# Performance work log

Hardware: AMD Instinct MI355X
Metric: run time of the kernel (lower is better)

## Reference

```python
import jax, jax.numpy as jnp
import numpy as np

N, T, CIN = 40000, 32, 8
VW = 64          # back_voxelwise_channels
P = 16           # v2b_maxvoxels (voxels stacked per BEV cell)
BEV_H, BEV_W = 496, 432
EPS = 1e-5


def _bn(key, shape):
    # returns stacked (gamma, beta, running_mean, running_var) along axis -2
    k1, k2, k3 = jax.random.split(key, 3)
    g = 1.0 + 0.1 * jax.random.normal(k1, shape, jnp.float32)
    b = 0.1 * jax.random.normal(k2, shape, jnp.float32)
    m = 0.1 * jax.random.normal(k3, shape, jnp.float32)
    v = jnp.ones(shape, jnp.float32)
    return jnp.stack([g, b, m, v], axis=-2)


def setup_inputs() -> dict:
    key = jax.random.key(0)
    ks = jax.random.split(key, 20)
    features = jax.random.normal(ks[0], (N, T, CIN), jnp.float32)
    cy = jax.random.randint(ks[1], (N, 1), 0, BEV_H)
    cx = jax.random.randint(ks[2], (N, 1), 0, BEV_W)
    coors = jnp.concatenate([cy, cx], axis=1).astype(jnp.int32)
    num_voxels = jax.random.randint(ks[3], (N,), 1, T + 1).astype(jnp.int32)

    def w(k, o, i):
        return jax.random.normal(k, (o, i), jnp.float32) / float(np.sqrt(i))

    return dict(
        features=features, coors=coors, num_voxels=num_voxels,
        vfe1_W=w(ks[4], 8, CIN), vfe1_bn=_bn(ks[5], (8,)),
        vfe2_W=w(ks[6], 32, 16), vfe2_bn=_bn(ks[7], (32,)),
        vfe3_W=w(ks[8], 64, 64), vfe3_bn=_bn(ks[9], (64,)),
        vfe4_W=w(ks[10], 64, 64), vfe4_bn=_bn(ks[11], (64,)),
        bfe1_W=jax.random.normal(ks[12], (16, P, P), jnp.float32) / float(np.sqrt(P)),
        bfe1_bn=_bn(ks[13], (16, P)),
        bfe2_W=jax.random.normal(ks[14], (16, 2, P), jnp.float32) / float(np.sqrt(P)),
        bfe2_bn=_bn(ks[15], (16, 2)),
        bfe3_W=w(ks[16], 128, 128), bfe3_bn=_bn(ks[17], (128,)),
    )


def _forward(features, vfe1_W, vfe1_bn, vfe2_W, vfe2_bn, vfe3_W, vfe3_bn,
             vfe4_W, vfe4_bn, bfe1_W, bfe1_bn, bfe2_W, bfe2_bn, bfe3_W, bfe3_bn,
             coors, num_voxels):
    n, t = features.shape[0], features.shape[1]
    f32 = features.dtype
    mask = (jnp.arange(t)[None, :] < num_voxels[:, None]).astype(f32)[..., None]  # [N,T,1]

    def fe(x, W, bn):  # Linear (no bias) + BatchNorm1d (eval) + Mish
        g, b, m, v = bn
        y = x @ W.T
        y = (y - m) * jax.lax.rsqrt(v + EPS) * g + b
        return y * jnp.tanh(jax.nn.softplus(y))

    def vfe(x, W, bn):  # pointwise FE, max-pool over points, concat
        p = fe(x, W, bn)
        agg = jnp.max(p, axis=1, keepdims=True)
        return jnp.concatenate([p, jnp.broadcast_to(agg, p.shape)], axis=2)

    x1 = vfe(features, vfe1_W, vfe1_bn)           # [N,T,16]
    x2 = vfe(x1, vfe2_W, vfe2_bn) * mask          # [N,T,64]
    x3 = fe(x2, vfe3_W, vfe3_bn)
    x4 = fe(x3, vfe4_W, vfe4_bn) * mask + x2
    voxelwise = jnp.max(x4, axis=1)               # [N,64]

    # ---- voxel2bev: group voxels by BEV cell, stack up to P per cell ----
    cell = coors[:, 0] * BEV_W + coors[:, 1]                         # [N]
    ucell, inv = jnp.unique(cell, return_inverse=True, size=n, fill_value=BEV_H * BEV_W)
    order = jnp.argsort(inv)                                          # stable
    inv_sorted = inv[order]
    pos_sorted = jnp.arange(n) - jnp.searchsorted(inv_sorted, inv_sorted, side='left')
    slot = jnp.zeros(n, jnp.int32).at[order].set(pos_sorted.astype(jnp.int32))
    row = jnp.where(slot < P, inv, n)                                 # overflow -> dropped
    bevs = jnp.zeros((n, P, VW), f32).at[row, jnp.minimum(slot, P - 1)].set(
        voxelwise, mode='drop')                                       # [N,P,64]
    counts = jax.ops.segment_sum(jnp.ones(n, jnp.int32), inv, num_segments=n)
    numv = jnp.minimum(counts, P)
    bevcoors = jnp.stack([ucell // BEV_W, ucell % BEV_W], axis=1)     # [N,2]

    # ---- 16 grouped FE stacks over the slot dimension ----
    x0 = bevs.transpose(0, 2, 1).reshape(n, 16, 4, P)                 # [N,16,4,P]
    m2 = (jnp.arange(P)[None, :] < numv[:, None]).astype(f32)[:, None, None, :]
    y = jnp.einsum('ngip,gqp->ngiq', x0, bfe1_W)                      # [N,16,4,P]
    g1, b1, m1, v1 = (bfe1_bn[None, :, i, None, :] for i in range(4))
    y = (y - m1) * jax.lax.rsqrt(v1 + EPS) * g1 + b1
    y = y * jnp.tanh(jax.nn.softplus(y)) * m2
    z = jnp.einsum('ngip,gcp->ngic', y, bfe2_W)                       # [N,16,4,2]
    g2, b2, m2b, v2 = (bfe2_bn[None, :, i, None, :] for i in range(4))
    z = (z - m2b) * jax.lax.rsqrt(v2 + EPS) * g2 + b2
    z = z * jnp.tanh(jax.nn.softplus(z))
    # torch cat along dim=-1 then view -> layout [N, 4, 16, 2] flattened
    x17 = z.transpose(0, 2, 1, 3).reshape(n, 128)
    x18 = fe(x17, bfe3_W, bfe3_bn)
    x19 = fe(x18, bfe3_W, bfe3_bn)   # original applies bfe3 twice (bfe4 unused)

    bevmap = jnp.zeros((BEV_H, BEV_W, 128), f32).at[
        bevcoors[:, 0], bevcoors[:, 1]].set(x19, mode='drop')
    return bevmap.transpose(2, 1, 0)                                  # [128, W, H]


def reference(features, coors, num_voxels, vfe1_W, vfe1_bn, vfe2_W, vfe2_bn,
              vfe3_W, vfe3_bn, vfe4_W, vfe4_bn, bfe1_W, bfe1_bn, bfe2_W, bfe2_bn,
              bfe3_W, bfe3_bn):
    return _forward(features, vfe1_W, vfe1_bn, vfe2_W, vfe2_bn, vfe3_W, vfe3_bn,
                    vfe4_W, vfe4_bn, bfe1_W, bfe1_bn, bfe2_W, bfe2_bn,
                    bfe3_W, bfe3_bn, coors, num_voxels)
```

## Files before the change

kernel.cpp:

```cpp
#include <hip/hip_runtime.h>

#define BEVW 432
#define BEVH 496
#define NCELL (BEVW*BEVH)
#define NVOX  40000
#define EPSB  1e-5f

typedef float f32x2 __attribute__((ext_vector_type(2)));
typedef float f32x4 __attribute__((ext_vector_type(4)));
typedef unsigned int u32x4 __attribute__((ext_vector_type(4)));
typedef short bf16x8 __attribute__((ext_vector_type(8)));

#define REP8_0(M)  M(0) M(1) M(2) M(3) M(4) M(5) M(6) M(7)
#define REP8_8(M)  M(8) M(9) M(10) M(11) M(12) M(13) M(14) M(15)
#define REP8_16(M) M(16) M(17) M(18) M(19) M(20) M(21) M(22) M(23)
#define REP8_24(M) M(24) M(25) M(26) M(27) M(28) M(29) M(30) M(31)
#define REP16_0(M)  REP8_0(M)  REP8_8(M)
#define REP32_0(M) REP16_0(M) REP8_16(M) REP8_24(M)


__device__ __forceinline__ float mishf(float y) {
    float e = __expf(fminf(y, 40.f));
    float n = e * (e + 2.f);
    return y * n * __builtin_amdgcn_rcpf(n + 2.f);
}

template <int CTRL>
__device__ __forceinline__ float dppmaxf(float a) {
    int p = __builtin_amdgcn_update_dpp(0, __float_as_int(a), CTRL, 0xF, 0xF, true);
    return fmaxf(a, __int_as_float(p));
}
#define WMAX32(a) { \
    a = dppmaxf<0xB1>(a); \
    a = dppmaxf<0x4E>(a); \
    a = dppmaxf<0x141>(a); \
    a = dppmaxf<0x140>(a); \
    a = fmaxf(a, __int_as_float(__builtin_amdgcn_ds_swizzle(__float_as_int(a), 0x401F))); }

__device__ __forceinline__ bf16x8 mkbf8(uint a, uint b, uint c, uint d) {
    u32x4 t = {a, b, c, d};
    return __builtin_bit_cast(bf16x8, t);
}

__device__ __forceinline__ uint splitbf(float x) {
    uint ux = __float_as_uint(x);
    uint rh = (ux + 0x7FFFu + ((ux >> 16) & 1u)) & 0xFFFF0000u;
    float lof = x - __uint_as_float(rh);
    uint ul = __float_as_uint(lof);
    uint rl = (ul + 0x7FFFu + ((ul >> 16) & 1u)) >> 16;
    return (rh >> 16) | (rl << 16);
}

__global__ __launch_bounds__(256) void setup_kernel(
    const float* __restrict__ vbn1, const float* __restrict__ vbn2,
    const float* __restrict__ vbn3, const float* __restrict__ vbn4,
    const float* __restrict__ bbn1, const float* __restrict__ bbn2,
    const float* __restrict__ bbn3, const float* __restrict__ W4,
    float* __restrict__ fold, ushort* __restrict__ w4fh, ushort* __restrict__ w4fl)
{
    int tid = threadIdx.x;
    if (tid < 8)  { float s = vbn1[tid]/sqrtf(vbn1[24+tid]+EPSB);  fold[tid]      = s; fold[8+tid]   = vbn1[8+tid]  - vbn1[16+tid]*s; }
    if (tid < 32) { float s = vbn2[tid]/sqrtf(vbn2[96+tid]+EPSB);  fold[16+tid]   = s; fold[48+tid]  = vbn2[32+tid] - vbn2[64+tid]*s; }
    if (tid < 64) { float s = vbn3[tid]/sqrtf(vbn3[192+tid]+EPSB); fold[80+tid]   = s; fold[144+tid] = vbn3[64+tid] - vbn3[128+tid]*s; }
    if (tid < 64) { float s = vbn4[tid]/sqrtf(vbn4[192+tid]+EPSB); fold[208+tid]  = s; fold[272+tid] = vbn4[64+tid] - vbn4[128+tid]*s; }
    if (tid < 128){ float s = bbn3[tid]/sqrtf(bbn3[384+tid]+EPSB); fold[336+tid]  = s; fold[464+tid] = bbn3[128+tid]- bbn3[256+tid]*s; }
    { int g = tid >> 4, q = tid & 15;
      const float* b = bbn1 + g*64;
      float s = b[q]/sqrtf(b[48+q]+EPSB);
      fold[592+tid] = s; fold[848+tid] = b[16+q] - b[32+q]*s; }
    if (tid < 32) { int g = tid >> 1, c = tid & 1;
      const float* b = bbn2 + g*8;
      float s = b[c]/sqrtf(b[6+c]+EPSB);
      fold[1104+tid] = s; fold[1136+tid] = b[2+c] - b[4+c]*s; }

    for (int i = tid; i < 4096; i += 256) {
        int j = i & 7, ln = (i >> 3) & 63, nt = (i >> 9) & 3, kc = i >> 11;
        int n = (ln & 15) + nt*16;
        int k = kc*32 + (ln >> 4)*8 + j;
        float val = W4[n*64 + k];
        uint ux = __float_as_uint(val);
        uint rh = (ux + 0x7FFFu + ((ux >> 16) & 1u)) & 0xFFFF0000u;
        float lof = val - __uint_as_float(rh);
        uint ul = __float_as_uint(lof);
        uint rl = (ul + 0x7FFFu + ((ul >> 16) & 1u)) >> 16;
        w4fh[i] = (ushort)(rh >> 16);
        w4fl[i] = (ushort)rl;
    }
}

#define PAIRS(M) M(0,0,1) M(1,2,3) M(2,4,5) M(3,6,7) M(4,8,9) M(5,10,11) \
  M(6,12,13) M(7,14,15) M(8,16,17) M(9,18,19) M(10,20,21) M(11,22,23) \
  M(12,24,25) M(13,26,27) M(14,28,29) M(15,30,31)

#define MF3(D, AH, AL, BH, BL) \
    D = __builtin_amdgcn_mfma_f32_16x16x32_bf16(AL, BH, D, 0, 0, 0); \
    D = __builtin_amdgcn_mfma_f32_16x16x32_bf16(AH, BL, D, 0, 0, 0); \
    D = __builtin_amdgcn_mfma_f32_16x16x32_bf16(AH, BH, D, 0, 0, 0);

__global__ __launch_bounds__(256, 3) void vfe_kernel(
    const float* __restrict__ feat, const int* __restrict__ coors,
    const int* __restrict__ nvx,
    const float* __restrict__ W1, const float* __restrict__ W2,
    const float* __restrict__ W3,
    const ushort* __restrict__ w4fh, const ushort* __restrict__ w4fl,
    const float* __restrict__ fold,
    float* __restrict__ voxelwise, int* __restrict__ cnt,
    int* __restrict__ list, int* __restrict__ nact, int* __restrict__ act)
{
    __shared__ char ldsbuf[4*8704];
    int tid = threadIdx.x;
    int lane = tid & 63;
    int wv = tid >> 6;
    int quad = lane >> 4;
    int v = blockIdx.x * 8 + (tid >> 5);
    int vA = blockIdx.x * 8 + 2*wv;
    int t = tid & 31;
    uint*  x3w  = (uint*)(ldsbuf + wv*8704);
    float* xw   = (float*)x3w;
    float* aggL = (float*)(ldsbuf + wv*8704 + 8448);

    const float* fp = feat + (v*32 + t)*8;
    float4 fa = *(const float4*)fp;
    float4 fb = *(const float4*)(fp+4);
    int numv = nvx[v];
    float maskf = (t < numv) ? 1.f : 0.f;

#define D1(o) float x1_##o; float m1_##o;
    REP8_0(D1)
#undef D1
#define FE1(o) { const float* w = W1 + (o)*8; \
    float ya = fa.x*w[0] + fa.y*w[1]; float yb = fa.z*w[2] + fa.w*w[3]; \
    float yc = fb.x*w[4] + fb.y*w[5]; float yd = fb.z*w[6] + fb.w*w[7]; \
    float yy = ((ya+yb)+(yc+yd)) * fold[(o)] + fold[8+(o)]; \
    x1_##o = mishf(yy); }
    REP8_0(FE1)
#undef FE1
#define P1(o) { float a = x1_##o; WMAX32(a); m1_##o = a; }
    REP8_0(P1)
#undef P1

    f32x2 x1p_0 = {x1_0,x1_1}, x1p_1 = {x1_2,x1_3}, x1p_2 = {x1_4,x1_5}, x1p_3 = {x1_6,x1_7};
    f32x2 m1p_0 = {m1_0,m1_1}, m1p_1 = {m1_2,m1_3}, m1p_2 = {m1_4,m1_5}, m1p_3 = {m1_6,m1_7};

#define D2(o) float x2_##o; float agg_##o;
    REP32_0(D2)
#undef D2
#define FE2(o) { const f32x2* wp = (const f32x2*)(W2 + (o)*16); \
    f32x2 sa = x1p_0*wp[0]; sa += x1p_1*wp[1]; \
    f32x2 sb = x1p_2*wp[2]; sb += x1p_3*wp[3]; \
    f32x2 sc = m1p_0*wp[4]; sc += m1p_1*wp[5]; \
    f32x2 sd = m1p_2*wp[6]; sd += m1p_3*wp[7]; \
    sa += sb; sc += sd; sa += sc; \
    float yy = (sa.x + sa.y) * fold[16+(o)] + fold[48+(o)]; \
    x2_##o = mishf(yy); }
    REP32_0(FE2)
#undef FE2
#define P2(o) { float a = x2_##o; WMAX32(a); agg_##o = a; }
    REP32_0(P2)
#undef P2

#define PX(i,a,b) f32x2 x2p_##i = {x2_##a, x2_##b}; f32x2 aggp_##i = {agg_##a, agg_##b};
    PAIRS(PX)
#undef PX

    const f32x2* wap = (const f32x2*)(W3 + t*64 + 32);
    const f32x2* wbp = (const f32x2*)(W3 + (t+32)*64 + 32);
    f32x2 yp1 = {0.f,0.f}, yp2 = {0.f,0.f};
#define YG(i) yp1 += aggp_##i * wap[i]; yp2 += aggp_##i * wbp[i];
    REP16_0(YG)
#undef YG
    float yagg1 = yp1.x + yp1.y, yagg2 = yp2.x + yp2.y;

    f32x2 maskp = {maskf, maskf};
#define MSK(i) x2p_##i *= maskp; aggp_##i *= maskp;
    REP16_0(MSK)
#undef MSK

    if (t == 0) {
        float* ag = aggL + (lane >> 5)*32;
#define AGW(i) ag[2*(i)] = aggp_##i.x; ag[2*(i)+1] = aggp_##i.y;
        REP16_0(AGW)
#undef AGW
    }

    int nA = __shfl(numv, 0);
    int nB = __shfl(numv, 32);

#define DD(i) f32x4 d_##i = {0.f,0.f,0.f,0.f};
    REP16_0(DD)
#undef DD

    for (int kc = 0; kc < 2; kc++) {
        float ysrc = kc ? yagg2 : yagg1;
        for (int o = 0; o < 32; o++) {
            int og = kc*32 + o;
            const f32x2* wp = (const f32x2*)(W3 + og*64);
            f32x2 s0 = x2p_0*wp[0];  s0 += x2p_1*wp[1];  s0 += x2p_2*wp[2];  s0 += x2p_3*wp[3];
            f32x2 s1 = x2p_4*wp[4];  s1 += x2p_5*wp[5];  s1 += x2p_6*wp[6];  s1 += x2p_7*wp[7];
            f32x2 s2 = x2p_8*wp[8];  s2 += x2p_9*wp[9];  s2 += x2p_10*wp[10]; s2 += x2p_11*wp[11];
            f32x2 s3 = x2p_12*wp[12]; s3 += x2p_13*wp[13]; s3 += x2p_14*wp[14]; s3 += x2p_15*wp[15];
            s0 += s1; s2 += s3; s0 += s2;
            float ya = __shfl(ysrc, o, 32);
            float yy = (s0.x + s0.y) + maskf * ya;
            yy = yy * fold[80+og] + fold[144+og];
            x3w[lane*33 + o] = splitbf(mishf(yy));
        }
        __syncthreads();

        const uint4* bh = (const uint4*)w4fh + (kc*4)*64 + lane;
        const uint4* bl = (const uint4*)w4fl + (kc*4)*64 + lane;

#define MFNT(D, nt) { \
    uint4 h = bh[(nt)*64]; uint4 l = bl[(nt)*64]; \
    bf16x8 Bh = mkbf8(h.x,h.y,h.z,h.w); bf16x8 Bl = mkbf8(l.x,l.y,l.z,l.w); \
    MF3(D, Ah, Al, Bh, Bl) }

#define DOMT(mt, D0, D1, D2, D3) { \
    int aoff = ((lane & 15) + 16*(mt))*33 + quad*8; \
    uint u0 = x3w[aoff+0], u1 = x3w[aoff+1], u2 = x3w[aoff+2], u3 = x3w[aoff+3]; \
    uint u4 = x3w[aoff+4], u5 = x3w[aoff+5], u6 = x3w[aoff+6], u7 = x3w[aoff+7]; \
    bf16x8 Ah = mkbf8(__builtin_amdgcn_perm(u1,u0,0x05040100), __builtin_amdgcn_perm(u3,u2,0x05040100), \
                      __builtin_amdgcn_perm(u5,u4,0x05040100), __builtin_amdgcn_perm(u7,u6,0x05040100)); \
    bf16x8 Al = mkbf8(__builtin_amdgcn_perm(u1,u0,0x07060302), __builtin_amdgcn_perm(u3,u2,0x07060302), \
                      __builtin_amdgcn_perm(u5,u4,0x07060302), __builtin_amdgcn_perm(u7,u6,0x07060302)); \
    MFNT(d_##D0, 0) MFNT(d_##D1, 1) MFNT(d_##D2, 2) MFNT(d_##D3, 3) }

        DOMT(0, 0, 1, 2, 3)
        DOMT(1, 4, 5, 6, 7)
        DOMT(2, 8, 9, 10, 11)
        DOMT(3, 12, 13, 14, 15)
#undef DOMT
#undef MFNT
        __syncthreads();
    }

#define XWR(i) xw[lane*33 + 2*(i)] = x2p_##i.x; xw[lane*33 + 2*(i)+1] = x2p_##i.y;
    REP16_0(XWR)
#undef XWR
    __syncthreads();

    int c0 = lane & 15;
    float s0f = fold[208+c0],    t0f = fold[272+c0];
    float s1f = fold[208+16+c0], t1f = fold[272+16+c0];
    float s2f = fold[208+32+c0], t2f = fold[272+32+c0];
    float s3f = fold[208+48+c0], t3f = fold[272+48+c0];
    float rA2 = aggL[c0],      rA3 = aggL[16+c0];
    float rB2 = aggL[32+c0],   rB3 = aggL[48+c0];
    float pA0=-3.4e38f, pA1=-3.4e38f, pA2=-3.4e38f, pA3=-3.4e38f;
    float pB0=-3.4e38f, pB1=-3.4e38f, pB2=-3.4e38f, pB3=-3.4e38f;

#define FTP(D, mt, nt, SS, TT, PV) { \
    int nv = ((mt) >> 1) ? nB : nA; \
    int rf = quad*4 + 16*(mt); \
    int rt = quad*4 + 16*((mt)&1); \
    int cb = c0 + 16*(nt); \
    float m0=(rt+0<nv)?1.f:0.f, m1=(rt+1<nv)?1.f:0.f, m2=(rt+2<nv)?1.f:0.f, m3=(rt+3<nv)?1.f:0.f; \
    float y0 = mishf(D.x*SS + TT)*m0 + xw[(rf+0)*33 + cb]; \
    float y1 = mishf(D.y*SS + TT)*m1 + xw[(rf+1)*33 + cb]; \
    float y2 = mishf(D.z*SS + TT)*m2 + xw[(rf+2)*33 + cb]; \
    float y3 = mishf(D.w*SS + TT)*m3 + xw[(rf+3)*33 + cb]; \
    PV = fmaxf(PV, fmaxf(fmaxf(y0,y1), fmaxf(y2,y3))); }

#define FTA(D, mt, nt, SS, TT, AG, PV) { \
    int nv = ((mt) >> 1) ? nB : nA; \
    int rt = quad*4 + 16*((mt)&1); \
    float m0=(rt+0<nv)?1.f:0.f, m1=(rt+1<nv)?1.f:0.f, m2=(rt+2<nv)?1.f:0.f, m3=(rt+3<nv)?1.f:0.f; \
    float y0 = (mishf(D.x*SS + TT) + AG)*m0; \
    float y1 = (mishf(D.y*SS + TT) + AG)*m1; \
    float y2 = (mishf(D.z*SS + TT) + AG)*m2; \
    float y3 = (mishf(D.w*SS + TT) + AG)*m3; \
    PV = fmaxf(PV, fmaxf(fmaxf(y0,y1), fmaxf(y2,y3))); }

    FTP(d_0, 0, 0, s0f, t0f, pA0)  FTP(d_1, 0, 1, s1f, t1f, pA1)
    FTA(d_2, 0, 2, s2f, t2f, rA2, pA2)  FTA(d_3, 0, 3, s3f, t3f, rA3, pA3)
    FTP(d_4, 1, 0, s0f, t0f, pA0)  FTP(d_5, 1, 1, s1f, t1f, pA1)
    FTA(d_6, 1, 2, s2f, t2f, rA2, pA2)  FTA(d_7, 1, 3, s3f, t3f, rA3, pA3)
    FTP(d_8, 2, 0, s0f, t0f, pB0)  FTP(d_9, 2, 1, s1f, t1f, pB1)
    FTA(d_10, 2, 2, s2f, t2f, rB2, pB2)  FTA(d_11, 2, 3, s3f, t3f, rB3, pB3)
    FTP(d_12, 3, 0, s0f, t0f, pB0)  FTP(d_13, 3, 1, s1f, t1f, pB1)
    FTA(d_14, 3, 2, s2f, t2f, rB2, pB2)  FTA(d_15, 3, 3, s3f, t3f, rB3, pB3)
#undef FTP
#undef FTA

#define RED(p) p = fmaxf(p, __shfl_xor(p, 16)); p = fmaxf(p, __shfl_xor(p, 32));
    RED(pA0) RED(pA1) RED(pA2) RED(pA3) RED(pB0) RED(pB1) RED(pB2) RED(pB3)
#undef RED

    if (quad == 0) {
        float* vwA = voxelwise + vA*64;
        vwA[c0] = pA0; vwA[c0+16] = pA1; vwA[c0+32] = pA2; vwA[c0+48] = pA3;
        float* vwB = voxelwise + (vA+1)*64;
        vwB[c0] = pB0; vwB[c0+16] = pB1; vwB[c0+32] = pB2; vwB[c0+48] = pB3;
    }

    if (t == 0) {
        int cell = coors[v*2] * BEVW + coors[v*2+1];
        int pos = atomicAdd(&cnt[cell], 1);
        if (pos < 16) list[cell*16 + pos] = v;
        if (pos == 0) { int k = atomicAdd(nact, 1); act[k] = cell; }
    }
}

__global__ __launch_bounds__(256) void bfe_front(
    const int* __restrict__ nact, const int* __restrict__ act,
    const int* __restrict__ cnt, const int* __restrict__ list,
    const float* __restrict__ voxelwise,
    const float* __restrict__ W1g, const float* __restrict__ W2g,
    const float* __restrict__ fold, float* __restrict__ x17g,
    int* __restrict__ idx)
{
    int n_act = *nact;
    int aidx = blockIdx.x * 4 + (threadIdx.x >> 6);
    if (aidx >= n_act) return;

    int lane = threadIdx.x & 63;
    int g = lane >> 2, ii = lane & 3;
    int cell = act[aidx];
    int numv = min(cnt[cell], 16);
    if (lane == 0) idx[cell] = aidx;

    int myidx = (lane < numv) ? list[cell*16 + lane] : (0x40000000 + lane);
    int rank = 0;
    for (int j = 0; j < numv; j++) { int vj = __shfl(myidx, j); rank += (vj < myidx) ? 1 : 0; }
    if (lane >= numv) rank = lane;
    int sorted = __builtin_amdgcn_ds_permute(rank << 2, myidx);

#define YD(q) float y_##q = 0.f;
    REP16_0(YD)
#undef YD
    for (int p = 0; p < numv; p++) {
        int sv = __shfl(sorted, p);
        float val = voxelwise[sv*64 + lane];
        const float* w = W1g + g*256 + p;
#define BF1(q) y_##q += val * w[(q)*16];
        REP16_0(BF1)
#undef BF1
    }
#define BN1(q) { float yy = y_##q * fold[592 + g*16 + (q)] + fold[848 + g*16 + (q)]; \
    yy = mishf(yy); y_##q = ((q) < numv) ? yy : 0.f; }
    REP16_0(BN1)
#undef BN1

    float z0 = 0.f, z1 = 0.f;
#define BF2(p) z0 += y_##p * W2g[g*32 + (p)]; z1 += y_##p * W2g[g*32 + 16 + (p)];
    REP16_0(BF2)
#undef BF2
    z0 = mishf(z0 * fold[1104 + g*2 + 0] + fold[1136 + g*2 + 0]);
    z1 = mishf(z1 * fold[1104 + g*2 + 1] + fold[1136 + g*2 + 1]);

    int k0 = ii*32 + g*2;
    *(float2*)(x17g + aidx*128 + k0) = make_float2(z0, z1);
}

__global__ __launch_bounds__(512, 4) void bfe3_fused(
    const int* __restrict__ nactp,
    const float* __restrict__ W3, const float* __restrict__ fold,
    float* __restrict__ x17g)
{
    __shared__ float XL[64*128];
    int tid = threadIdx.x;
    int n_act = *nactp;
    int cb = blockIdx.x * 64;

    for (int i = tid; i < 64*32; i += 512) {
        int c = i >> 5, kc = i & 31;
        float4 val = (cb + c < n_act) ? ((const float4*)x17g)[(size_t)(cb+c)*32 + kc]
                                      : make_float4(0.f,0.f,0.f,0.f);
        ((float4*)XL)[c*32 + (kc ^ (c & 31))] = val;
    }
    __syncthreads();

    int wv = __builtin_amdgcn_readfirstlane(tid >> 6);
    int c  = tid & 63;
    int ob = wv * 16;
    int cswz = c & 31;
    const float4* xrow = (const float4*)XL + c*32;
    const float4* W4p = (const float4*)W3;

#define DECLB(q) f32x2 ap_##q = {0.f, 0.f};
#define ACCB(q) { const f32x2* wp_ = (const f32x2*)(W4p + (ob+(q))*32 + kc); \
    ap_##q += xv01 * wp_[0]; ap_##q += xv23 * wp_[1]; }
#define ACTB(q) float a_##q; { float yy = (ap_##q.x + ap_##q.y) * fold[336+ob+(q)] + fold[464+ob+(q)]; a_##q = mishf(yy); }
    {
        REP16_0(DECLB)
        for (int kc = 0; kc < 32; kc++) {
            float4 xv = xrow[kc ^ cswz];
            f32x2 xv01 = {xv.x, xv.y}, xv23 = {xv.z, xv.w};
            REP16_0(ACCB)
        }
        REP16_0(ACTB)
        __syncthreads();
        ((float4*)XL)[c*32 + ((wv*4 + 0) ^ cswz)] = make_float4(a_0,  a_1,  a_2,  a_3);
        ((float4*)XL)[c*32 + ((wv*4 + 1) ^ cswz)] = make_float4(a_4,  a_5,  a_6,  a_7);
        ((float4*)XL)[c*32 + ((wv*4 + 2) ^ cswz)] = make_float4(a_8,  a_9,  a_10, a_11);
        ((float4*)XL)[c*32 + ((wv*4 + 3) ^ cswz)] = make_float4(a_12, a_13, a_14, a_15);
    }
    __syncthreads();

    {
        const float4* yrow = (const float4*)XL + c*32;
        REP16_0(DECLB)
        for (int kc = 0; kc < 32; kc++) {
            float4 xv = yrow[kc ^ cswz];
            f32x2 xv01 = {xv.x, xv.y}, xv23 = {xv.z, xv.w};
            REP16_0(ACCB)
        }
        REP16_0(ACTB)
        float4* dst = (float4*)(x17g + (size_t)(cb + c)*128 + ob);
        dst[0] = make_float4(a_0,  a_1,  a_2,  a_3);
        dst[1] = make_float4(a_4,  a_5,  a_6,  a_7);
        dst[2] = make_float4(a_8,  a_9,  a_10, a_11);
        dst[3] = make_float4(a_12, a_13, a_14, a_15);
    }
#undef DECLB
#undef ACCB
#undef ACTB
}

__global__ __launch_bounds__(512, 2) void bev_write(
    const int* __restrict__ idx, const float* __restrict__ x19c,
    float* __restrict__ out)
{
    __shared__ float XT[128*65];
    int bid = blockIdx.x;
    int cx = bid % BEVW;
    int cy0 = (bid / BEVW) << 6;
    int tid = threadIdx.x;

    int cell_l = tid >> 3;
    int chq = (tid & 7) << 4;
    int cy = cy0 + cell_l;
    float4 v0 = make_float4(0.f,0.f,0.f,0.f), v1 = v0, v2 = v0, v3 = v0;
    if (cy < BEVH) {
        int ai = idx[cy*BEVW + cx];
        if (ai >= 0) {
            const float4* src = (const float4*)(x19c + (size_t)ai*128 + chq);
            v0 = src[0]; v1 = src[1]; v2 = src[2]; v3 = src[3];
        }
    }
    float* d = XT + chq*65 + cell_l;
    d[0*65]=v0.x;  d[1*65]=v0.y;  d[2*65]=v0.z;  d[3*65]=v0.w;
    d[4*65]=v1.x;  d[5*65]=v1.y;  d[6*65]=v1.z;  d[7*65]=v1.w;
    d[8*65]=v2.x;  d[9*65]=v2.y;  d[10*65]=v2.z; d[11*65]=v2.w;
    d[12*65]=v3.x; d[13*65]=v3.y; d[14*65]=v3.z; d[15*65]=v3.w;
    __syncthreads();

    int wv2 = tid >> 6, lane = tid & 63;
    int cyw = cy0 + lane;
    if (cyw < BEVH) {
        float* op = out + cx*BEVH + cyw;
#pragma unroll
        for (int k = 0; k < 16; k++) {
            int c = (wv2 << 4) + k;
            op[(size_t)c*NCELL] = XT[c*65 + lane];
        }
    }
}

extern "C" void kernel_launch(void* const* d_in, const int* in_sizes, int n_in,
                              void* d_out, int out_size, void* d_ws, size_t ws_size,
                              hipStream_t stream) {
    const float* features = (const float*)d_in[0];
    const int*   coors    = (const int*)d_in[1];
    const int*   num_vox  = (const int*)d_in[2];
    const float* vfe1_W   = (const float*)d_in[3];
    const float* vfe1_bn  = (const float*)d_in[4];
    const float* vfe2_W   = (const float*)d_in[5];
    const float* vfe2_bn  = (const float*)d_in[6];
    const float* vfe3_W   = (const float*)d_in[7];
    const float* vfe3_bn  = (const float*)d_in[8];
    const float* vfe4_W   = (const float*)d_in[9];
    const float* vfe4_bn  = (const float*)d_in[10];
    const float* bfe1_W   = (const float*)d_in[11];
    const float* bfe1_bn  = (const float*)d_in[12];
    const float* bfe2_W   = (const float*)d_in[13];
    const float* bfe2_bn  = (const float*)d_in[14];
    const float* bfe3_W   = (const float*)d_in[15];
    const float* bfe3_bn  = (const float*)d_in[16];
    float* out = (float*)d_out;

    char* ws = (char*)d_ws;
    int*    nact      = (int*)ws;
    int*    cnt       = (int*)(ws + 256);
    int*    list      = (int*)(ws + 857600);
    float*  voxelwise = (float*)(ws + 14571008);
    int*    act       = (int*)(ws + 24811008);
    float*  x17g      = (float*)(ws + 24971008);
    float*  fold      = (float*)(ws + 45451008);
    ushort* w4fh      = (ushort*)(ws + 45455680);
    ushort* w4fl      = (ushort*)(ws + 45463872);
    int*    idx       = (int*)(ws + 45472064);

    (void)hipMemsetAsync(ws, 0, 857600, stream);
    (void)hipMemsetAsync(idx, 0xFF, (size_t)NCELL*4, stream);

    setup_kernel<<<1, 256, 0, stream>>>(vfe1_bn, vfe2_bn, vfe3_bn, vfe4_bn,
                                        bfe1_bn, bfe2_bn, bfe3_bn, vfe4_W,
                                        fold, w4fh, w4fl);
    vfe_kernel<<<NVOX/8, 256, 0, stream>>>(features, coors, num_vox,
                                           vfe1_W, vfe2_W, vfe3_W, w4fh, w4fl, fold,
                                           voxelwise, cnt, list, nact, act);
    bfe_front<<<NVOX/4, 256, 0, stream>>>(nact, act, cnt, list, voxelwise,
                                          bfe1_W, bfe2_W, fold, x17g, idx);
    bfe3_fused<<<(NVOX+63)/64, 512, 0, stream>>>(nact, bfe3_W, fold, x17g);
    bev_write<<<BEVW*8, 512, 0, stream>>>(idx, x17g, out);
}
```

Baseline: 560.5 us.

## Compute vfe3 linear layer with split-bf16 MFMA instead of scalar FMA

The vfe3 64x64 linear layer, previously scalar f32x2 FMAs per thread with a shuffle-based aggregate term, now runs as split-bf16 (hi/lo, three MFMA) matrix multiplies over the x2 and aggregate halves staged in LDS. vfe3_W is pre-split in the setup kernel, and the results feed vfe4 MFMAs directly through an LDS staging area. The residual x2 values are rebuilt from the split representation. LDS per block roughly doubles and the launch bound drops to 2 blocks per CU, which lowers occupancy. The split-bf16 reconstruction also brings small precision differences.

```diff
diff --git a/kernel.cpp b/kernel.cpp
--- a/kernel.cpp
+++ b/kernel.cpp
@@ -56,7 +56,9 @@
     const float* __restrict__ vbn3, const float* __restrict__ vbn4,
     const float* __restrict__ bbn1, const float* __restrict__ bbn2,
     const float* __restrict__ bbn3, const float* __restrict__ W4,
-    float* __restrict__ fold, ushort* __restrict__ w4fh, ushort* __restrict__ w4fl)
+    const float* __restrict__ W3g,
+    float* __restrict__ fold, ushort* __restrict__ w4fh, ushort* __restrict__ w4fl,
+    ushort* __restrict__ w3fh, ushort* __restrict__ w3fl)
 {
     int tid = threadIdx.x;
     if (tid < 8)  { float s = vbn1[tid]/sqrtf(vbn1[24+tid]+EPSB);  fold[tid]      = s; fold[8+tid]   = vbn1[8+tid]  - vbn1[16+tid]*s; }
@@ -77,14 +79,26 @@
         int j = i & 7, ln = (i >> 3) & 63, nt = (i >> 9) & 3, kc = i >> 11;
         int n = (ln & 15) + nt*16;
         int k = kc*32 + (ln >> 4)*8 + j;
-        float val = W4[n*64 + k];
-        uint ux = __float_as_uint(val);
-        uint rh = (ux + 0x7FFFu + ((ux >> 16) & 1u)) & 0xFFFF0000u;
-        float lof = val - __uint_as_float(rh);
-        uint ul = __float_as_uint(lof);
-        uint rl = (ul + 0x7FFFu + ((ul >> 16) & 1u)) >> 16;
-        w4fh[i] = (ushort)(rh >> 16);
-        w4fl[i] = (ushort)rl;
+        {
+            float val = W4[n*64 + k];
+            uint ux = __float_as_uint(val);
+            uint rh = (ux + 0x7FFFu + ((ux >> 16) & 1u)) & 0xFFFF0000u;
+            float lof = val - __uint_as_float(rh);
+            uint ul = __float_as_uint(lof);
+            uint rl = (ul + 0x7FFFu + ((ul >> 16) & 1u)) >> 16;
+            w4fh[i] = (ushort)(rh >> 16);
+            w4fl[i] = (ushort)rl;
+        }
+        {
+            float val = W3g[n*64 + k];
+            uint ux = __float_as_uint(val);
+            uint rh = (ux + 0x7FFFu + ((ux >> 16) & 1u)) & 0xFFFF0000u;
+            float lof = val - __uint_as_float(rh);
+            uint ul = __float_as_uint(lof);
+            uint rl = (ul + 0x7FFFu + ((ul >> 16) & 1u)) >> 16;
+            w3fh[i] = (ushort)(rh >> 16);
+            w3fl[i] = (ushort)rl;
+        }
     }
 }
 
@@ -97,17 +111,30 @@
     D = __builtin_amdgcn_mfma_f32_16x16x32_bf16(AH, BL, D, 0, 0, 0); \
     D = __builtin_amdgcn_mfma_f32_16x16x32_bf16(AH, BH, D, 0, 0, 0);
 
-__global__ __launch_bounds__(256, 3) void vfe_kernel(
+#define DOMTX(SRCP, BHP, BLP, mt, D0, D1, D2, D3) { \
+    const uint* ap_ = (SRCP) + ((lane & 15) + 16*(mt))*33 + quad*8; \
+    uint u0 = ap_[0], u1 = ap_[1], u2 = ap_[2], u3 = ap_[3]; \
+    uint u4 = ap_[4], u5 = ap_[5], u6 = ap_[6], u7 = ap_[7]; \
+    bf16x8 Ah = mkbf8(__builtin_amdgcn_perm(u1,u0,0x05040100), __builtin_amdgcn_perm(u3,u2,0x05040100), \
+                      __builtin_amdgcn_perm(u5,u4,0x05040100), __builtin_amdgcn_perm(u7,u6,0x05040100)); \
+    bf16x8 Al = mkbf8(__builtin_amdgcn_perm(u1,u0,0x07060302), __builtin_amdgcn_perm(u3,u2,0x07060302), \
+                      __builtin_amdgcn_perm(u5,u4,0x07060302), __builtin_amdgcn_perm(u7,u6,0x07060302)); \
+    { uint4 h = (BHP)[0];   uint4 l = (BLP)[0];   bf16x8 Bh = mkbf8(h.x,h.y,h.z,h.w), Bl = mkbf8(l.x,l.y,l.z,l.w); MF3(D0, Ah, Al, Bh, Bl) } \
+    { uint4 h = (BHP)[64];  uint4 l = (BLP)[64];  bf16x8 Bh = mkbf8(h.x,h.y,h.z,h.w), Bl = mkbf8(l.x,l.y,l.z,l.w); MF3(D1, Ah, Al, Bh, Bl) } \
+    { uint4 h = (BHP)[128]; uint4 l = (BLP)[128]; bf16x8 Bh = mkbf8(h.x,h.y,h.z,h.w), Bl = mkbf8(l.x,l.y,l.z,l.w); MF3(D2, Ah, Al, Bh, Bl) } \
+    { uint4 h = (BHP)[192]; uint4 l = (BLP)[192]; bf16x8 Bh = mkbf8(h.x,h.y,h.z,h.w), Bl = mkbf8(l.x,l.y,l.z,l.w); MF3(D3, Ah, Al, Bh, Bl) } }
+
+__global__ __launch_bounds__(256, 2) void vfe_kernel(
     const float* __restrict__ feat, const int* __restrict__ coors,
     const int* __restrict__ nvx,
     const float* __restrict__ W1, const float* __restrict__ W2,
-    const float* __restrict__ W3,
+    const ushort* __restrict__ w3fh, const ushort* __restrict__ w3fl,
     const ushort* __restrict__ w4fh, const ushort* __restrict__ w4fl,
     const float* __restrict__ fold,
     float* __restrict__ voxelwise, int* __restrict__ cnt,
     int* __restrict__ list, int* __restrict__ nact, int* __restrict__ act)
 {
-    __shared__ char ldsbuf[4*8704];
+    __shared__ char ldsbuf[4*17152];
     int tid = threadIdx.x;
     int lane = tid & 63;
     int wv = tid >> 6;
@@ -115,9 +142,8 @@
     int v = blockIdx.x * 8 + (tid >> 5);
     int vA = blockIdx.x * 8 + 2*wv;
     int t = tid & 31;
-    uint*  x3w  = (uint*)(ldsbuf + wv*8704);
-    float* xw   = (float*)x3w;
-    float* aggL = (float*)(ldsbuf + wv*8704 + 8448);
+    uint*  x2s  = (uint*)(ldsbuf + wv*17152);
+    float* aggL = (float*)(ldsbuf + wv*17152 + 16896);
 
     const float* fp = feat + (v*32 + t)*8;
     float4 fa = *(const float4*)fp;
@@ -163,14 +189,6 @@
     PAIRS(PX)
 #undef PX
 
-    const f32x2* wap = (const f32x2*)(W3 + t*64 + 32);
-    const f32x2* wbp = (const f32x2*)(W3 + (t+32)*64 + 32);
-    f32x2 yp1 = {0.f,0.f}, yp2 = {0.f,0.f};
-#define YG(i) yp1 += aggp_##i * wap[i]; yp2 += aggp_##i * wbp[i];
-    REP16_0(YG)
-#undef YG
-    float yagg1 = yp1.x + yp1.y, yagg2 = yp2.x + yp2.y;
-
     f32x2 maskp = {maskf, maskf};
 #define MSK(i) x2p_##i *= maskp; aggp_##i *= maskp;
     REP16_0(MSK)
@@ -186,60 +204,76 @@
     int nA = __shfl(numv, 0);
     int nB = __shfl(numv, 32);
 
+#define X2W(i) { \
+    x2s[lane*33 + 2*(i)]          = splitbf(x2p_##i.x); \
+    x2s[lane*33 + 2*(i)+1]        = splitbf(x2p_##i.y); \
+    x2s[2112 + lane*33 + 2*(i)]   = splitbf(aggp_##i.x); \
+    x2s[2112 + lane*33 + 2*(i)+1] = splitbf(aggp_##i.y); }
+    REP16_0(X2W)
+#undef X2W
+
+#define E_DECL(i) f32x4 e_##i = {0.f,0.f,0.f,0.f};
+    REP16_0(E_DECL)
+#undef E_DECL
+    {
+        const uint4* bh3 = (const uint4*)w3fh + lane;
+        const uint4* bl3 = (const uint4*)w3fl + lane;
+        DOMTX(x2s, bh3, bl3, 0, e_0, e_1, e_2, e_3)
+        DOMTX(x2s, bh3, bl3, 1, e_4, e_5, e_6, e_7)
+        DOMTX(x2s, bh3, bl3, 2, e_8, e_9, e_10, e_11)
+        DOMTX(x2s, bh3, bl3, 3, e_12, e_13, e_14, e_15)
+    }
+    {
+        const uint4* bh3 = (const uint4*)w3fh + 256 + lane;
+        const uint4* bl3 = (const uint4*)w3fl + 256 + lane;
+        const uint* sp = x2s + 2112;
+        DOMTX(sp, bh3, bl3, 0, e_0, e_1, e_2, e_3)
+        DOMTX(sp, bh3, bl3, 1, e_4, e_5, e_6, e_7)
+        DOMTX(sp, bh3, bl3, 2, e_8, e_9, e_10, e_11)
+        DOMTX(sp, bh3, bl3, 3, e_12, e_13, e_14, e_15)
+    }
+
+    int c0 = lane & 15;
+    uint* x3st = x2s + 2112;
 #define DD(i) f32x4 d_##i = {0.f,0.f,0.f,0.f};
     REP16_0(DD)
 #undef DD
 
-    for (int kc = 0; kc < 2; kc++) {
-        float ysrc = kc ? yagg2 : yagg1;
-        for (int o = 0; o < 32; o++) {
-            int og = kc*32 + o;
-            const f32x2* wp = (const f32x2*)(W3 + og*64);
-            f32x2 s0 = x2p_0*wp[0];  s0 += x2p_1*wp[1];  s0 += x2p_2*wp[2];  s0 += x2p_3*wp[3];
-            f32x2 s1 = x2p_4*wp[4];  s1 += x2p_5*wp[5];  s1 += x2p_6*wp[6];  s1 += x2p_7*wp[7];
-            f32x2 s2 = x2p_8*wp[8];  s2 += x2p_9*wp[9];  s2 += x2p_10*wp[10]; s2 += x2p_11*wp[11];
-            f32x2 s3 = x2p_12*wp[12]; s3 += x2p_13*wp[13]; s3 += x2p_14*wp[14]; s3 += x2p_15*wp[15];
-            s0 += s1; s2 += s3; s0 += s2;
-            float ya = __shfl(ysrc, o, 32);
-            float yy = (s0.x + s0.y) + maskf * ya;
-            yy = yy * fold[80+og] + fold[144+og];
-            x3w[lane*33 + o] = splitbf(mishf(yy));
-        }
-        __syncthreads();
-
-        const uint4* bh = (const uint4*)w4fh + (kc*4)*64 + lane;
-        const uint4* bl = (const uint4*)w4fl + (kc*4)*64 + lane;
-
-#define MFNT(D, nt) { \
-    uint4 h = bh[(nt)*64]; uint4 l = bl[(nt)*64]; \
-    bf16x8 Bh = mkbf8(h.x,h.y,h.z,h.w); bf16x8 Bl = mkbf8(l.x,l.y,l.z,l.w); \
-    MF3(D, Ah, Al, Bh, Bl) }
-
-#define DOMT(mt, D0, D1, D2, D3) { \
-    int aoff = ((lane & 15) + 16*(mt))*33 + quad*8; \
-    uint u0 = x3w[aoff+0], u1 = x3w[aoff+1], u2 = x3w[aoff+2], u3 = x3w[aoff+3]; \
-    uint u4 = x3w[aoff+4], u5 = x3w[aoff+5], u6 = x3w[aoff+6], u7 = x3w[aoff+7]; \
-    bf16x8 Ah = mkbf8(__builtin_amdgcn_perm(u1,u0,0x05040100), __builtin_amdgcn_perm(u3,u2,0x05040100), \
-                      __builtin_amdgcn_perm(u5,u4,0x05040100), __builtin_amdgcn_perm(u7,u6,0x05040100)); \
-    bf16x8 Al = mkbf8(__builtin_amdgcn_perm(u1,u0,0x07060302), __builtin_amdgcn_perm(u3,u2,0x07060302), \
-                      __builtin_amdgcn_perm(u5,u4,0x07060302), __builtin_amdgcn_perm(u7,u6,0x07060302)); \
-    MFNT(d_##D0, 0) MFNT(d_##D1, 1) MFNT(d_##D2, 2) MFNT(d_##D3, 3) }
-
-        DOMT(0, 0, 1, 2, 3)
-        DOMT(1, 4, 5, 6, 7)
-        DOMT(2, 8, 9, 10, 11)
-        DOMT(3, 12, 13, 14, 15)
-#undef DOMT
-#undef MFNT
-        __syncthreads();
-    }
-
-#define XWR(i) xw[lane*33 + 2*(i)] = x2p_##i.x; xw[lane*33 + 2*(i)+1] = x2p_##i.y;
-    REP16_0(XWR)
-#undef XWR
-    __syncthreads();
-
-    int c0 = lane & 15;
+#define POST(TI, mt, nt) { \
+    float s_ = fold[80 + c0 + 16*(nt)], tb_ = fold[144 + c0 + 16*(nt)]; \
+    int col_ = c0 + 16*((nt)&1); \
+    int rowb_ = quad*4 + 16*(mt); \
+    x3st[(rowb_+0)*33 + col_] = splitbf(mishf(e_##TI.x * s_ + tb_)); \
+    x3st[(rowb_+1)*33 + col_] = splitbf(mishf(e_##TI.y * s_ + tb_)); \
+    x3st[(rowb_+2)*33 + col_] = splitbf(mishf(e_##TI.z * s_ + tb_)); \
+    x3st[(rowb_+3)*33 + col_] = splitbf(mishf(e_##TI.w * s_ + tb_)); }
+
+    {
+        POST(0,0,0)  POST(1,0,1)
+        POST(4,1,0)  POST(5,1,1)
+        POST(8,2,0)  POST(9,2,1)
+        POST(12,3,0) POST(13,3,1)
+        const uint4* bh4 = (const uint4*)w4fh + lane;
+        const uint4* bl4 = (const uint4*)w4fl + lane;
+        DOMTX(x3st, bh4, bl4, 0, d_0, d_1, d_2, d_3)
+        DOMTX(x3st, bh4, bl4, 1, d_4, d_5, d_6, d_7)
+        DOMTX(x3st, bh4, bl4, 2, d_8, d_9, d_10, d_11)
+        DOMTX(x3st, bh4, bl4, 3, d_12, d_13, d_14, d_15)
+    }
+    {
+        POST(2,0,2)  POST(3,0,3)
+        POST(6,1,2)  POST(7,1,3)
+        POST(10,2,2) POST(11,2,3)
+        POST(14,3,2) POST(15,3,3)
+        const uint4* bh4 = (const uint4*)w4fh + 256 + lane;
+        const uint4* bl4 = (const uint4*)w4fl + 256 + lane;
+        DOMTX(x3st, bh4, bl4, 0, d_0, d_1, d_2, d_3)
+        DOMTX(x3st, bh4, bl4, 1, d_4, d_5, d_6, d_7)
+        DOMTX(x3st, bh4, bl4, 2, d_8, d_9, d_10, d_11)
+        DOMTX(x3st, bh4, bl4, 3, d_12, d_13, d_14, d_15)
+    }
+#undef POST
+
     float s0f = fold[208+c0],    t0f = fold[272+c0];
     float s1f = fold[208+16+c0], t1f = fold[272+16+c0];
     float s2f = fold[208+32+c0], t2f = fold[272+32+c0];
@@ -249,16 +283,19 @@
     float pA0=-3.4e38f, pA1=-3.4e38f, pA2=-3.4e38f, pA3=-3.4e38f;
     float pB0=-3.4e38f, pB1=-3.4e38f, pB2=-3.4e38f, pB3=-3.4e38f;
 
+#define RECON(u) (__uint_as_float((u)<<16) + __uint_as_float((u) & 0xFFFF0000u))
 #define FTP(D, mt, nt, SS, TT, PV) { \
     int nv = ((mt) >> 1) ? nB : nA; \
     int rf = quad*4 + 16*(mt); \
     int rt = quad*4 + 16*((mt)&1); \
     int cb = c0 + 16*(nt); \
     float m0=(rt+0<nv)?1.f:0.f, m1=(rt+1<nv)?1.f:0.f, m2=(rt+2<nv)?1.f:0.f, m3=(rt+3<nv)?1.f:0.f; \
-    float y0 = mishf(D.x*SS + TT)*m0 + xw[(rf+0)*33 + cb]; \
-    float y1 = mishf(D.y*SS + TT)*m1 + xw[(rf+1)*33 + cb]; \
-    float y2 = mishf(D.z*SS + TT)*m2 + xw[(rf+2)*33 + cb]; \
-    float y3 = mishf(D.w*SS + TT)*m3 + xw[(rf+3)*33 + cb]; \
+    uint ua_ = x2s[(rf+0)*33 + cb], ub_ = x2s[(rf+1)*33 + cb]; \
+    uint uc_ = x2s[(rf+2)*33 + cb], ud_ = x2s[(rf+3)*33 + cb]; \
+    float y0 = mishf(D.x*SS + TT)*m0 + RECON(ua_); \
+    float y1 = mishf(D.y*SS + TT)*m1 + RECON(ub_); \
+    float y2 = mishf(D.z*SS + TT)*m2 + RECON(uc_); \
+    float y3 = mishf(D.w*SS + TT)*m3 + RECON(ud_); \
     PV = fmaxf(PV, fmaxf(fmaxf(y0,y1), fmaxf(y2,y3))); }
 
 #define FTA(D, mt, nt, SS, TT, AG, PV) { \
@@ -281,6 +318,7 @@
     FTA(d_14, 3, 2, s2f, t2f, rB2, pB2)  FTA(d_15, 3, 3, s3f, t3f, rB3, pB3)
 #undef FTP
 #undef FTA
+#undef RECON
 
 #define RED(p) p = fmaxf(p, __shfl_xor(p, 16)); p = fmaxf(p, __shfl_xor(p, 32));
     RED(pA0) RED(pA1) RED(pA2) RED(pA3) RED(pB0) RED(pB1) RED(pB2) RED(pB3)
@@ -490,15 +528,17 @@
     ushort* w4fh      = (ushort*)(ws + 45455680);
     ushort* w4fl      = (ushort*)(ws + 45463872);
     int*    idx       = (int*)(ws + 45472064);
+    ushort* w3fh      = (ushort*)(ws + 46329344);
+    ushort* w3fl      = (ushort*)(ws + 46337536);
 
     (void)hipMemsetAsync(ws, 0, 857600, stream);
     (void)hipMemsetAsync(idx, 0xFF, (size_t)NCELL*4, stream);
 
     setup_kernel<<<1, 256, 0, stream>>>(vfe1_bn, vfe2_bn, vfe3_bn, vfe4_bn,
-                                        bfe1_bn, bfe2_bn, bfe3_bn, vfe4_W,
-                                        fold, w4fh, w4fl);
+                                        bfe1_bn, bfe2_bn, bfe3_bn, vfe4_W, vfe3_W,
+                                        fold, w4fh, w4fl, w3fh, w3fl);
     vfe_kernel<<<NVOX/8, 256, 0, stream>>>(features, coors, num_vox,
-                                           vfe1_W, vfe2_W, vfe3_W, w4fh, w4fl, fold,
+                                           vfe1_W, vfe2_W, w3fh, w3fl, w4fh, w4fl, fold,
                                            voxelwise, cnt, list, nact, act);
     bfe_front<<<NVOX/4, 256, 0, stream>>>(nact, act, cnt, list, voxelwise,
                                           bfe1_W, bfe2_W, fold, x17g, idx);
```

Measured after the change: 525.6 us. 6.2% less time.
